# Kernel optimization log

Measured on AMD Instinct MI355X. Metric: run time of the kernel, lower is better.

Reference implementation:

```python
import jax, jax.numpy as jnp
import numpy as np

SR = 48000
TIME_LENGTH = 62400  # int(1.3 * 48000)
MAX_VOICES = 16


def _conv1d_same(x, k, b):
    # x: [B, L, Cin], k: [K, Cin, Cout] -> [B, L, Cout], keras Conv1D padding='same'
    y = jax.lax.conv_general_dilated(x, k, (1,), 'SAME', dimension_numbers=('NWC', 'WIO', 'NWC'))
    return y + b


def setup_inputs() -> dict:
    key = jax.random.key(0)
    ks = jax.random.split(key, 20)
    B, L, D, C = 16, 250, 128, 32
    V = MAX_VOICES
    din = D + C
    w = lambda k, s: jax.random.normal(k, s, jnp.float32) * 0.05
    inp = {}
    inp['base_signal'] = jax.random.normal(ks[0], (B, TIME_LENGTH), jnp.float32)
    inp['z'] = jax.random.normal(ks[1], (B, L, D), jnp.float32)
    inp['cond'] = jax.random.uniform(ks[2], (B, C), jnp.float32)
    inp['fundamental_freq'] = jax.random.uniform(ks[3], (B,), jnp.float32)
    # param_predictor: Dense(256)->Dense(128)->Dense(64)->Dense(4)
    inp['W1'] = w(ks[4], (din, 256)); inp['b1'] = jnp.zeros((256,), jnp.float32)
    inp['W2'] = w(ks[5], (256, 128)); inp['b2'] = jnp.zeros((128,), jnp.float32)
    inp['W3'] = w(ks[6], (128, 64));  inp['b3'] = jnp.zeros((64,), jnp.float32)
    inp['W4'] = w(ks[7], (64, 4));    inp['b4'] = jnp.zeros((4,), jnp.float32)
    # voice_gain_net: Conv1D(128,7)->Conv1D(64,5)->Conv1D(V,3), input channels = D + C
    inp['K1'] = w(ks[8], (7, din, 128)); inp['cb1'] = jnp.zeros((128,), jnp.float32)
    inp['K2'] = w(ks[9], (5, 128, 64));  inp['cb2'] = jnp.zeros((64,), jnp.float32)
    inp['K3'] = w(ks[10], (3, 64, V));   inp['cb3'] = jnp.zeros((V,), jnp.float32)
    return inp


def reference(base_signal, z, cond, fundamental_freq,
              W1, b1, W2, b2, W3, b3, W4, b4,
              K1, cb1, K2, cb2, K3, cb3):
    B, T = base_signal.shape
    L = z.shape[1]
    V = MAX_VOICES
    # ---- global param predictor ----
    z_global = jnp.mean(z, axis=1)
    x = jnp.concatenate([z_global, cond], axis=-1)
    h = jax.nn.relu(x @ W1 + b1)
    h = jax.nn.relu(h @ W2 + b2)
    h = jax.nn.relu(h @ W3 + b3)
    params = h @ W4 + b4  # [B,4]
    num_voices = 1.0 + 14.0 * jax.nn.sigmoid(params[:, 0:1])  # [B,1]
    detune_cents = params[:, 1:2] * 50.0                       # [B,1] (unused downstream, as in source)
    spread = jax.nn.sigmoid(params[:, 2:3])                    # [B,1]
    depth = jax.nn.sigmoid(params[:, 3:4]) * 0.5               # [B,1]
    # ---- per-voice gain envelopes at latent rate ----
    z_cond = jnp.concatenate([z, jnp.broadcast_to(cond[:, None, :], (B, L, cond.shape[-1]))], axis=-1)
    g = jax.nn.relu(_conv1d_same(z_cond, K1, cb1))
    g = jax.nn.relu(_conv1d_same(g, K2, cb2))
    g = _conv1d_same(g, K3, cb3)  # [B, L, V]
    # TF bilinear resize (half-pixel centers) L -> T along time axis
    scale = L / T
    src = jnp.clip((jnp.arange(T, dtype=jnp.float32) + 0.5) * scale - 0.5, 0.0, L - 1.0)
    i0 = jnp.floor(src).astype(jnp.int32)
    i1 = jnp.minimum(i0 + 1, L - 1)
    frac = (src - i0.astype(jnp.float32))[None, :, None]
    vg = g[:, i0, :] * (1.0 - frac) + g[:, i1, :] * frac
    voice_gains = jax.nn.softplus(vg)  # [B, T, V]
    # ---- 16-voice detune/roll/LFO-modulate/accumulate, vectorized over voices ----
    pos = (np.arange(V) - (V - 1) / 2.0) / V            # static [V]
    shifts = np.trunc(pos * 20.0).astype(np.int64)      # int() truncation as in source
    gidx = (np.arange(T)[None, :] - shifts[:, None]) % T  # static [V, T] gather for tf.roll
    shifted = base_signal[:, jnp.asarray(gidx)]         # [B, V, T]
    t = jnp.arange(T, dtype=jnp.float32) / SR
    lfo_freq = 3.0 + 0.3 * jnp.arange(V, dtype=jnp.float32)
    lfo = jnp.sin(2.0 * np.pi * lfo_freq[:, None] * t[None, :])  # [V, T]
    modulated = shifted * (1.0 + 0.2 * depth[:, 0][:, None, None] * lfo[None])  # [B, V, T]
    pan = 1.0 - jnp.abs(jnp.asarray(pos, dtype=jnp.float32))[None, :] * spread * 0.5  # [B, V]
    unison = jnp.einsum('bvt,btv,bv->bt', modulated, voice_gains, pan)  # [B, T]
    # ---- soft voice-count mask and normalization ----
    voice_mask = jax.nn.sigmoid((num_voices - jnp.arange(V, dtype=jnp.float32)[None, :]) * 2.0)  # [B, V]
    norm = jnp.sqrt(jnp.sum(voice_mask, axis=-1, keepdims=True) + 1e-6)  # [B, 1]
    gain_sum = jnp.einsum('btv,bv->bt', voice_gains, voice_mask)  # [B, T]
    return gain_sum / (norm + 1e-6) * unison
```

## Files before the change

kernel.cpp:

```cpp
#include <hip/hip_runtime.h>
#include <hip/hip_bf16.h>
#include <math.h>

#define L_LEN 250
#define D_DIM 128
#define C_DIM 32
#define DIN   160
#define NV    16
#define T_LEN 62400
#define CB    244

__global__ __launch_bounds__(256) void conv1_mlp_kernel(
        const float* __restrict__ z, const float* __restrict__ cond,
        const float* __restrict__ K1, float* __restrict__ parts1,
        const float* __restrict__ W1, const float* __restrict__ b1,
        const float* __restrict__ W2, const float* __restrict__ b2,
        const float* __restrict__ W3, const float* __restrict__ b3,
        const float* __restrict__ W4, const float* __restrict__ b4,
        float* __restrict__ P) {
    int tid = threadIdx.x;
    if (blockIdx.x < 16) {
        int b = blockIdx.x;
        __shared__ float xb[DIN];
        __shared__ float4 sm4[8][32];
        __shared__ float h1[256];
        __shared__ float h2[128];
        __shared__ float h3[64];
        __shared__ float pr[4];
        {
            int c4 = tid & 31, rg = tid >> 5;
            const float4* zp = (const float4*)(z + (size_t)b * L_LEN * D_DIM) + c4;
            float4 acc = make_float4(0.f, 0.f, 0.f, 0.f);
            for (int r = rg; r < L_LEN; r += 8) {
                float4 v = zp[(size_t)r * 32];
                acc.x += v.x; acc.y += v.y; acc.z += v.z; acc.w += v.w;
            }
            sm4[rg][c4] = acc;
        }
        __syncthreads();
        if (tid < 32) {
            float4 acc = sm4[0][tid];
            #pragma unroll
            for (int g = 1; g < 8; ++g) {
                float4 v = sm4[g][tid];
                acc.x += v.x; acc.y += v.y; acc.z += v.z; acc.w += v.w;
            }
            const float inv = 1.0f / (float)L_LEN;
            acc.x *= inv; acc.y *= inv; acc.z *= inv; acc.w *= inv;
            ((float4*)xb)[tid] = acc;
        } else if (tid >= 128 && tid < DIN) {
            xb[tid] = cond[b * C_DIM + (tid - 128)];
        }
        __syncthreads();
        {
            float a0 = b1[tid], a1 = 0.f;
            #pragma unroll 8
            for (int i = 0; i < DIN; i += 2) {
                a0 = fmaf(xb[i],     W1[i * 256 + tid],       a0);
                a1 = fmaf(xb[i + 1], W1[(i + 1) * 256 + tid], a1);
            }
            h1[tid] = fmaxf(a0 + a1, 0.f);
        }
        __syncthreads();
        if (tid < 128) {
            float a0 = b2[tid], a1 = 0.f;
            #pragma unroll 8
            for (int i = 0; i < 256; i += 2) {
                a0 = fmaf(h1[i],     W2[i * 128 + tid],       a0);
                a1 = fmaf(h1[i + 1], W2[(i + 1) * 128 + tid], a1);
            }
            h2[tid] = fmaxf(a0 + a1, 0.f);
        }
        __syncthreads();
        if (tid < 64) {
            float a0 = b3[tid], a1 = 0.f;
            #pragma unroll 8
            for (int i = 0; i < 128; i += 2) {
                a0 = fmaf(h2[i],     W3[i * 64 + tid],       a0);
                a1 = fmaf(h2[i + 1], W3[(i + 1) * 64 + tid], a1);
            }
            h3[tid] = fmaxf(a0 + a1, 0.f);
        }
        __syncthreads();
        if (tid < 4) {
            float acc = b4[tid];
            #pragma unroll 8
            for (int i = 0; i < 64; ++i) acc = fmaf(h3[i], W4[i * 4 + tid], acc);
            pr[tid] = acc;
        }
        __syncthreads();
        if (tid == 0) {
            float num_voices = 1.0f + 14.0f / (1.0f + __expf(-pr[0]));
            float spread     = 1.0f / (1.0f + __expf(-pr[2]));
            float depth      = 0.5f / (1.0f + __expf(-pr[3]));
            float* Pb = P + b * 40;
            float msum = 0.f;
            for (int v = 0; v < NV; ++v) {
                float m = 1.0f / (1.0f + __expf(-(num_voices - (float)v) * 2.0f));
                msum += m;
                Pb[2 + v] = m;
                float pos = ((float)v - 7.5f) * (1.0f / 16.0f);
                Pb[2 + NV + v] = 1.0f - fabsf(pos) * spread * 0.5f;
            }
            float norm = sqrtf(msum + 1e-6f);
            Pb[0] = depth;
            Pb[1] = 1.0f / (norm + 1e-6f);
        }
        return;
    }
    int blk = blockIdx.x - 16;
    int s  = blk >> 8;
    int b  = (blk >> 4) & 15;
    int lt = blk & 15;
    int l0 = lt * 16;
    __shared__ float smc[40][28];
    for (int idx = tid; idx < 22 * 40; idx += 256) {
        int pl = idx / 40;
        int il = idx - pl * 40;
        int p  = l0 - 3 + pl;
        int gi = s * 40 + il;
        float v = 0.f;
        if (p >= 0 && p < L_LEN)
            v = (gi < D_DIM) ? z[((size_t)b * L_LEN + p) * D_DIM + gi]
                             : cond[b * C_DIM + (gi - D_DIM)];
        smc[il][pl] = v;
    }
    __syncthreads();
    int oc = tid & 127;
    int lb = (tid >> 7) * 8;
    float acc[8];
    #pragma unroll
    for (int j = 0; j < 8; ++j) acc[j] = 0.f;
    const float* kbase = K1 + (size_t)(s * 40) * 128 + oc;
    for (int il = 0; il < 40; ++il) {
        float zr[16];
        *(float4*)&zr[0]  = *(const float4*)&smc[il][lb];
        *(float4*)&zr[4]  = *(const float4*)&smc[il][lb + 4];
        *(float4*)&zr[8]  = *(const float4*)&smc[il][lb + 8];
        *(float4*)&zr[12] = *(const float4*)&smc[il][lb + 12];
        const float* kp = kbase + (size_t)il * 128;
        #pragma unroll
        for (int tap = 0; tap < 7; ++tap) {
            float k = kp[(size_t)tap * DIN * 128];
            #pragma unroll
            for (int j = 0; j < 8; ++j) acc[j] = fmaf(zr[tap + j], k, acc[j]);
        }
    }
    float* po = parts1 + (size_t)s * (16 * L_LEN * 128) + ((size_t)b * L_LEN) * 128 + oc;
    #pragma unroll
    for (int j = 0; j < 8; ++j) {
        int l = l0 + lb + j;
        if (l < L_LEN) po[(size_t)l * 128] = acc[j];
    }
}

__global__ __launch_bounds__(256) void conv2_split_kernel(
        const float* __restrict__ parts1, const float* __restrict__ cb1,
        const float* __restrict__ K2, float* __restrict__ parts2) {
    int blk = blockIdx.x;
    int h  = blk >> 8;
    int b  = (blk >> 4) & 15;
    int lt = blk & 15;
    int l0 = lt * 16;
    int tid = threadIdx.x;
    const int PSTR = 16 * L_LEN * 128;
    __shared__ float sm[64][28];
    for (int idx = tid; idx < 20 * 64; idx += 256) {
        int pl = idx >> 6;
        int il = idx & 63;
        int p  = l0 - 2 + pl;
        int gi = h * 64 + il;
        float v = 0.f;
        if (p >= 0 && p < L_LEN) {
            size_t o = ((size_t)b * L_LEN + p) * 128 + gi;
            v = cb1[gi] + parts1[o] + parts1[o + PSTR] + parts1[o + 2 * PSTR] + parts1[o + 3 * PSTR];
            v = fmaxf(v, 0.f);
        }
        sm[il][pl] = v;
    }
    __syncthreads();
    int oc = tid & 63;
    int lb = (tid >> 6) * 4;
    float acc[4];
    #pragma unroll
    for (int j = 0; j < 4; ++j) acc[j] = 0.f;
    const float* kbase = K2 + (size_t)(h * 64) * 64 + oc;
    for (int il = 0; il < 64; ++il) {
        float zr[8];
        *(float4*)&zr[0] = *(const float4*)&sm[il][lb];
        *(float4*)&zr[4] = *(const float4*)&sm[il][lb + 4];
        const float* kp = kbase + (size_t)il * 64;
        #pragma unroll
        for (int tap = 0; tap < 5; ++tap) {
            float k = kp[(size_t)tap * 128 * 64];
            #pragma unroll
            for (int j = 0; j < 4; ++j) acc[j] = fmaf(zr[tap + j], k, acc[j]);
        }
    }
    float* po = parts2 + (size_t)h * (16 * L_LEN * 64) + ((size_t)b * L_LEN) * 64 + oc;
    #pragma unroll
    for (int j = 0; j < 4; ++j) {
        int l = l0 + lb + j;
        if (l < L_LEN) po[(size_t)l * 64] = acc[j];
    }
}

__global__ __launch_bounds__(256) void conv3_main_kernel(
        const float* __restrict__ base, const float* __restrict__ parts2,
        const float* __restrict__ cb2,
        const float* __restrict__ K3, const float* __restrict__ cb3,
        const float* __restrict__ P, float* __restrict__ out) {
    int b = blockIdx.x / CB;
    int c = blockIdx.x % CB;
    int t0 = c * 256;
    int tid = threadIdx.x;
    const int PSTR2 = 16 * L_LEN * 64;
    const float scale = 250.0f / 62400.0f;

    __shared__ float k3t[16][196];
    __shared__ float sA[6][68];
    __shared__ float g3loc[4][17];
    __shared__ float Pb[34];

    float src0 = ((float)t0 + 0.5f) * scale - 0.5f;
    src0 = fminf(fmaxf(src0, 0.0f), 249.0f);
    int L0 = (int)floorf(src0);

    if (tid < 34) Pb[tid] = P[b * 40 + tid];
    for (int idx = tid; idx < 3 * 64 * 16; idx += 256) {
        int v  = idx & 15;
        int ti = idx >> 4;
        k3t[v][ti] = K3[ti * 16 + v];
    }
    for (int idx = tid; idx < 6 * 64; idx += 256) {
        int pl = idx >> 6;
        int i  = idx & 63;
        int p  = L0 - 1 + pl;
        float v = 0.f;
        if (p >= 0 && p < L_LEN) {
            size_t o = ((size_t)b * L_LEN + p) * 64 + i;
            v = fmaxf(cb2[i] + parts2[o] + parts2[o + PSTR2], 0.f);
        }
        sA[pl][i] = v;
    }
    __syncthreads();

    {
        int seg = tid & 3;
        int v   = (tid >> 2) & 15;
        int r   = tid >> 6;
        float acc = 0.f;
        #pragma unroll
        for (int tap = 0; tap < 3; ++tap) {
            const float* gr = &sA[r + tap][seg * 16];
            const float* kr = &k3t[v][tap * 64 + seg * 16];
            #pragma unroll
            for (int j = 0; j < 4; ++j) {
                float4 g = *(const float4*)&gr[j * 4];
                float4 k = *(const float4*)&kr[j * 4];
                acc = fmaf(g.x, k.x, acc);
                acc = fmaf(g.y, k.y, acc);
                acc = fmaf(g.z, k.z, acc);
                acc = fmaf(g.w, k.w, acc);
            }
        }
        acc += __shfl_xor(acc, 1);
        acc += __shfl_xor(acc, 2);
        if (seg == 0) g3loc[r][v] = acc + cb3[v];
    }
    __syncthreads();

    int t = t0 + tid;
    if (t >= T_LEN) return;
    float depth = Pb[0];
    float coef  = Pb[1];
    float src = ((float)t + 0.5f) * scale - 0.5f;
    src = fminf(fmaxf(src, 0.0f), 249.0f);
    float fi0 = floorf(src);
    int i0 = (int)fi0;
    int i1 = min(i0 + 1, L_LEN - 1);
    float frac = src - fi0;
    int r0 = i0 - L0;
    int r1 = i1 - L0;
    float vg[16];
    #pragma unroll
    for (int v = 0; v < NV; ++v) {
        float a = g3loc[r0][v];
        float d = g3loc[r1][v];
        vg[v] = fmaf(d - a, frac, a);
    }
    float tsec = (float)t * (1.0f / 48000.0f);
    const float* bs = base + (size_t)b * T_LEN;
    const int shifts[NV] = {-9,-8,-6,-5,-4,-3,-1,0,0,1,3,4,5,6,8,9};
    float gain_sum = 0.f, uni = 0.f;
    #pragma unroll
    for (int v = 0; v < NV; ++v) {
        float x = vg[v];
        float sp = fmaxf(x, 0.f) + __logf(1.0f + __expf(-fabsf(x)));
        float fv = 3.0f + 0.3f * (float)v;
        float ph = fv * tsec;
        ph -= floorf(ph);
        float lfo = __builtin_amdgcn_sinf(ph);
        int tb = t - shifts[v];
        if (tb < 0) tb += T_LEN; else if (tb >= T_LEN) tb -= T_LEN;
        float mod = bs[tb] * fmaf(0.2f * depth, lfo, 1.0f);
        gain_sum = fmaf(sp, Pb[2 + v], gain_sum);
        uni      = fmaf(mod * sp, Pb[2 + NV + v], uni);
    }
    out[(size_t)b * T_LEN + t] = gain_sum * coef * uni;
}

__global__ void params_kernel(const float* __restrict__ z, const float* __restrict__ cond,
                              const float* __restrict__ W1, const float* __restrict__ b1,
                              const float* __restrict__ W2, const float* __restrict__ b2,
                              const float* __restrict__ W3, const float* __restrict__ b3,
                              const float* __restrict__ W4, const float* __restrict__ b4,
                              float* __restrict__ P) {
    int b = blockIdx.x;
    int tid = threadIdx.x;
    __shared__ float xb[DIN];
    __shared__ float zp2[128];
    __shared__ float h1[256];
    __shared__ float h2[128];
    __shared__ float h3[64];
    __shared__ float pr[4];
    {
        int i = tid & 127, half = tid >> 7;
        const float* zp = z + (size_t)b * L_LEN * D_DIM + i;
        float s = 0.f;
        for (int l = half; l < L_LEN; l += 2) s += zp[(size_t)l * D_DIM];
        if (half) zp2[i] = s;
        __syncthreads();
        if (!half) xb[i] = (s + zp2[i]) * (1.0f / (float)L_LEN);
        if (tid >= 128 && tid < DIN) xb[tid] = cond[b * C_DIM + (tid - 128)];
    }
    __syncthreads();
    {
        float acc = b1[tid];
        for (int i = 0; i < DIN; ++i) acc = fmaf(xb[i], W1[i * 256 + tid], acc);
        h1[tid] = fmaxf(acc, 0.f);
    }
    __syncthreads();
    if (tid < 128) {
        float acc = b2[tid];
        for (int i = 0; i < 256; ++i) acc = fmaf(h1[i], W2[i * 128 + tid], acc);
        h2[tid] = fmaxf(acc, 0.f);
    }
    __syncthreads();
    if (tid < 64) {
        float acc = b3[tid];
        for (int i = 0; i < 128; ++i) acc = fmaf(h2[i], W3[i * 64 + tid], acc);
        h3[tid] = fmaxf(acc, 0.f);
    }
    __syncthreads();
    if (tid < 4) {
        float acc = b4[tid];
        for (int i = 0; i < 64; ++i) acc = fmaf(h3[i], W4[i * 4 + tid], acc);
        pr[tid] = acc;
    }
    __syncthreads();
    if (tid == 0) {
        float num_voices = 1.0f + 14.0f / (1.0f + __expf(-pr[0]));
        float spread     = 1.0f / (1.0f + __expf(-pr[2]));
        float depth      = 0.5f / (1.0f + __expf(-pr[3]));
        float* Pb = P + b * 40;
        float msum = 0.f;
        for (int v = 0; v < NV; ++v) {
            float m = 1.0f / (1.0f + __expf(-(num_voices - (float)v) * 2.0f));
            msum += m;
            Pb[2 + v] = m;
            float pos = ((float)v - 7.5f) * (1.0f / 16.0f);
            Pb[2 + NV + v] = 1.0f - fabsf(pos) * spread * 0.5f;
        }
        float norm = sqrtf(msum + 1e-6f);
        Pb[0] = depth;
        Pb[1] = 1.0f / (norm + 1e-6f);
    }
}

__global__ void conv1_mono_kernel(const float* __restrict__ z, const float* __restrict__ cond,
                                  const float* __restrict__ K1, const float* __restrict__ cb1,
                                  float* __restrict__ g1) {
    int b  = blockIdx.x >> 4;
    int lt = blockIdx.x & 15;
    int l0 = lt * 16;
    int tid = threadIdx.x;
    __shared__ float sm[DIN][22];
    for (int idx = tid; idx < 22 * DIN; idx += 256) {
        int pl = idx / DIN;
        int i  = idx - pl * DIN;
        int p  = l0 - 3 + pl;
        float v = 0.f;
        if (p >= 0 && p < L_LEN)
            v = (i < D_DIM) ? z[((size_t)b * L_LEN + p) * D_DIM + i]
                            : cond[b * C_DIM + (i - D_DIM)];
        sm[i][pl] = v;
    }
    __syncthreads();
    int oc = tid & 127;
    int lb = (tid >> 7) * 8;
    float bias = cb1[oc];
    float acc[8];
    #pragma unroll
    for (int j = 0; j < 8; ++j) acc[j] = bias;
    for (int i = 0; i < DIN; ++i) {
        float zr[14];
        #pragma unroll
        for (int q = 0; q < 14; ++q) zr[q] = sm[i][lb + q];
        #pragma unroll
        for (int tap = 0; tap < 7; ++tap) {
            float k = K1[(size_t)(tap * DIN + i) * 128 + oc];
            #pragma unroll
            for (int j = 0; j < 8; ++j) acc[j] = fmaf(zr[tap + j], k, acc[j]);
        }
    }
    #pragma unroll
    for (int j = 0; j < 8; ++j) {
        int l = l0 + lb + j;
        if (l < L_LEN) g1[((size_t)b * L_LEN + l) * 128 + oc] = fmaxf(acc[j], 0.f);
    }
}

__global__ void conv2_mono_kernel(const float* __restrict__ g1,
                                  const float* __restrict__ K2, const float* __restrict__ cb2,
                                  float* __restrict__ g2) {
    int b  = blockIdx.x >> 4;
    int lt = blockIdx.x & 15;
    int l0 = lt * 16;
    int tid = threadIdx.x;
    __shared__ float sm[128][20];
    for (int idx = tid; idx < 20 * 128; idx += 256) {
        int pl = idx >> 7;
        int i  = idx & 127;
        int p  = l0 - 2 + pl;
        float v = (p >= 0 && p < L_LEN) ? g1[((size_t)b * L_LEN + p) * 128 + i] : 0.f;
        sm[i][pl] = v;
    }
    __syncthreads();
    int oc = tid & 63;
    int lb = (tid >> 6) * 4;
    float bias = cb2[oc];
    float acc[4];
    #pragma unroll
    for (int j = 0; j < 4; ++j) acc[j] = bias;
    for (int i = 0; i < 128; ++i) {
        float zr[8];
        #pragma unroll
        for (int q = 0; q < 8; ++q) zr[q] = sm[i][lb + q];
        #pragma unroll
        for (int tap = 0; tap < 5; ++tap) {
            float k = K2[(size_t)(tap * 128 + i) * 64 + oc];
            #pragma unroll
            for (int j = 0; j < 4; ++j) acc[j] = fmaf(zr[tap + j], k, acc[j]);
        }
    }
    #pragma unroll
    for (int j = 0; j < 4; ++j) {
        int l = l0 + lb + j;
        if (l < L_LEN) g2[((size_t)b * L_LEN + l) * 64 + oc] = fmaxf(acc[j], 0.f);
    }
}

__global__ void conv3_mono_kernel(const float* __restrict__ g2,
                                  const float* __restrict__ K3, const float* __restrict__ cb3,
                                  float* __restrict__ g3) {
    int b  = blockIdx.x >> 4;
    int lt = blockIdx.x & 15;
    int l0 = lt * 16;
    int tid = threadIdx.x;
    int v  = tid & 15;
    int ll = tid >> 4;
    int l  = l0 + ll;
    if (l >= L_LEN) return;
    float acc = cb3[v];
    #pragma unroll
    for (int tap = 0; tap < 3; ++tap) {
        int p = l + tap - 1;
        if (p < 0 || p >= L_LEN) continue;
        const float* gp = g2 + ((size_t)b * L_LEN + p) * 64;
        #pragma unroll
        for (int i = 0; i < 64; ++i) acc = fmaf(gp[i], K3[(size_t)(tap * 64 + i) * 16 + v], acc);
    }
    g3[((size_t)b * L_LEN + l) * 16 + v] = acc;
}

__global__ __launch_bounds__(256) void main_mono_kernel(
        const float* __restrict__ base, const float* __restrict__ g3,
        const float* __restrict__ P, float* __restrict__ out) {
    int b = blockIdx.x / CB;
    int c = blockIdx.x % CB;
    int t = c * 256 + threadIdx.x;
    __shared__ float Pb[34];
    if (threadIdx.x < 34) Pb[threadIdx.x] = P[b * 40 + threadIdx.x];
    __syncthreads();
    if (t >= T_LEN) return;
    float depth = Pb[0];
    float coef  = Pb[1];
    const float scale = 250.0f / 62400.0f;
    float src = ((float)t + 0.5f) * scale - 0.5f;
    src = fminf(fmaxf(src, 0.0f), 249.0f);
    float fi0 = floorf(src);
    int i0 = (int)fi0;
    int i1 = min(i0 + 1, L_LEN - 1);
    float frac = src - fi0;
    const float4* r0 = (const float4*)(g3 + ((size_t)b * L_LEN + i0) * NV);
    const float4* r1 = (const float4*)(g3 + ((size_t)b * L_LEN + i1) * NV);
    float vg[16];
    #pragma unroll
    for (int q = 0; q < 4; ++q) {
        float4 a = r0[q];
        float4 d = r1[q];
        vg[q * 4 + 0] = fmaf(d.x - a.x, frac, a.x);
        vg[q * 4 + 1] = fmaf(d.y - a.y, frac, a.y);
        vg[q * 4 + 2] = fmaf(d.z - a.z, frac, a.z);
        vg[q * 4 + 3] = fmaf(d.w - a.w, frac, a.w);
    }
    float tsec = (float)t * (1.0f / 48000.0f);
    const float* bs = base + (size_t)b * T_LEN;
    const int shifts[NV] = {-9,-8,-6,-5,-4,-3,-1,0,0,1,3,4,5,6,8,9};
    float gain_sum = 0.f, uni = 0.f;
    #pragma unroll
    for (int v = 0; v < NV; ++v) {
        float x = vg[v];
        float sp = fmaxf(x, 0.f) + __logf(1.0f + __expf(-fabsf(x)));
        float fv = 3.0f + 0.3f * (float)v;
        float ph = fv * tsec;
        ph -= floorf(ph);
        float lfo = __builtin_amdgcn_sinf(ph);
        int tb = t - shifts[v];
        if (tb < 0) tb += T_LEN; else if (tb >= T_LEN) tb -= T_LEN;
        float mod = bs[tb] * fmaf(0.2f * depth, lfo, 1.0f);
        gain_sum = fmaf(sp, Pb[2 + v], gain_sum);
        uni      = fmaf(mod * sp, Pb[2 + NV + v], uni);
    }
    out[(size_t)b * T_LEN + t] = gain_sum * coef * uni;
}

extern "C" void kernel_launch(void* const* d_in, const int* in_sizes, int n_in,
                              void* d_out, int out_size, void* d_ws, size_t ws_size,
                              hipStream_t stream) {
    const float* base = (const float*)d_in[0];
    const float* z    = (const float*)d_in[1];
    const float* cond = (const float*)d_in[2];
    const float* W1 = (const float*)d_in[4];  const float* b1 = (const float*)d_in[5];
    const float* W2 = (const float*)d_in[6];  const float* b2 = (const float*)d_in[7];
    const float* W3 = (const float*)d_in[8];  const float* b3 = (const float*)d_in[9];
    const float* W4 = (const float*)d_in[10]; const float* b4 = (const float*)d_in[11];
    const float* K1 = (const float*)d_in[12]; const float* cb1 = (const float*)d_in[13];
    const float* K2 = (const float*)d_in[14]; const float* cb2 = (const float*)d_in[15];
    const float* K3 = (const float*)d_in[16]; const float* cb3 = (const float*)d_in[17];
    float* out = (float*)d_out;

    int B = in_sizes[0] / T_LEN;

    float* ws = (float*)d_ws;
    const size_t P1 = (size_t)16 * L_LEN * 128;
    const size_t P2 = (size_t)16 * L_LEN * 64;
    size_t need = (1024 + 4 * P1 + 2 * P2) * sizeof(float);

    float* P = ws;
    if (ws_size >= need) {
        float* parts1 = ws + 1024;
        float* parts2 = parts1 + 4 * P1;
        conv1_mlp_kernel<<<16 + 4 * B * 16, 256, 0, stream>>>(
            z, cond, K1, parts1, W1, b1, W2, b2, W3, b3, W4, b4, P);
        conv2_split_kernel<<<2 * B * 16, 256, 0, stream>>>(parts1, cb1, K2, parts2);
        conv3_main_kernel<<<B * CB, 256, 0, stream>>>(base, parts2, cb2, K3, cb3, P, out);
    } else {
        float* g1 = ws + 1024;
        float* g2 = g1 + (size_t)B * L_LEN * 128;
        float* g3 = g2 + (size_t)B * L_LEN * 64;
        params_kernel<<<B, 256, 0, stream>>>(z, cond, W1, b1, W2, b2, W3, b3, W4, b4, P);
        conv1_mono_kernel<<<B * 16, 256, 0, stream>>>(z, cond, K1, cb1, g1);
        conv2_mono_kernel<<<B * 16, 256, 0, stream>>>(g1, K2, cb2, g2);
        conv3_mono_kernel<<<B * 16, 256, 0, stream>>>(g2, K3, cb3, g3);
        main_mono_kernel<<<B * CB, 256, 0, stream>>>(base, g3, P, out);
    }
}
```

Measured before the change: 65.28 us.

## Register-tile conv1/conv2 over output channel pairs and split conv2 input four ways

Conv1 and conv2 now give each thread two adjacent output channels and fewer positions. Weights are loaded as float2 and two input channels are processed per iteration, so each shared-memory input value feeds more FMAs. Conv2 splits its input channels four ways instead of two, doubling its block count for more parallelism. Conv3 therefore sums four partial buffers, and the workspace requirement grows.

```diff
diff --git a/kernel.cpp b/kernel.cpp
--- a/kernel.cpp
+++ b/kernel.cpp
@@ -113,7 +113,7 @@
     int b  = (blk >> 4) & 15;
     int lt = blk & 15;
     int l0 = lt * 16;
-    __shared__ float smc[40][28];
+    __shared__ float smc[40][24];
     for (int idx = tid; idx < 22 * 40; idx += 256) {
         int pl = idx / 40;
         int il = idx - pl * 40;
@@ -126,31 +126,44 @@
         smc[il][pl] = v;
     }
     __syncthreads();
-    int oc = tid & 127;
-    int lb = (tid >> 7) * 8;
-    float acc[8];
-    #pragma unroll
-    for (int j = 0; j < 8; ++j) acc[j] = 0.f;
-    const float* kbase = K1 + (size_t)(s * 40) * 128 + oc;
-    for (int il = 0; il < 40; ++il) {
-        float zr[16];
-        *(float4*)&zr[0]  = *(const float4*)&smc[il][lb];
-        *(float4*)&zr[4]  = *(const float4*)&smc[il][lb + 4];
-        *(float4*)&zr[8]  = *(const float4*)&smc[il][lb + 8];
-        *(float4*)&zr[12] = *(const float4*)&smc[il][lb + 12];
-        const float* kp = kbase + (size_t)il * 128;
+    int oc0   = (tid & 63) << 1;
+    int lbase = (tid >> 6) * 4;
+    float acc[2][4];
+    #pragma unroll
+    for (int j = 0; j < 4; ++j) { acc[0][j] = 0.f; acc[1][j] = 0.f; }
+    const float* kb = K1 + (size_t)(s * 40) * 128 + oc0;
+    for (int il = 0; il < 40; il += 2) {
+        float2 w0[7], w1[7];
         #pragma unroll
         for (int tap = 0; tap < 7; ++tap) {
-            float k = kp[(size_t)tap * DIN * 128];
+            const float* k0 = kb + ((size_t)tap * DIN + il) * 128;
+            w0[tap] = *(const float2*)(k0);
+            w1[tap] = *(const float2*)(k0 + 128);
+        }
+        float zr0[10], zr1[10];
+        *(float4*)&zr0[0] = *(const float4*)&smc[il][lbase];
+        *(float4*)&zr0[4] = *(const float4*)&smc[il][lbase + 4];
+        *(float2*)&zr0[8] = *(const float2*)&smc[il][lbase + 8];
+        *(float4*)&zr1[0] = *(const float4*)&smc[il + 1][lbase];
+        *(float4*)&zr1[4] = *(const float4*)&smc[il + 1][lbase + 4];
+        *(float2*)&zr1[8] = *(const float2*)&smc[il + 1][lbase + 8];
+        #pragma unroll
+        for (int tap = 0; tap < 7; ++tap) {
             #pragma unroll
-            for (int j = 0; j < 8; ++j) acc[j] = fmaf(zr[tap + j], k, acc[j]);
-        }
-    }
-    float* po = parts1 + (size_t)s * (16 * L_LEN * 128) + ((size_t)b * L_LEN) * 128 + oc;
-    #pragma unroll
-    for (int j = 0; j < 8; ++j) {
-        int l = l0 + lb + j;
-        if (l < L_LEN) po[(size_t)l * 128] = acc[j];
+            for (int j = 0; j < 4; ++j) {
+                acc[0][j] = fmaf(zr0[tap + j], w0[tap].x, acc[0][j]);
+                acc[1][j] = fmaf(zr0[tap + j], w0[tap].y, acc[1][j]);
+                acc[0][j] = fmaf(zr1[tap + j], w1[tap].x, acc[0][j]);
+                acc[1][j] = fmaf(zr1[tap + j], w1[tap].y, acc[1][j]);
+            }
+        }
+    }
+    float* po = parts1 + (size_t)s * (16 * L_LEN * 128)
+              + ((size_t)b * L_LEN + l0 + lbase) * 128 + oc0;
+    #pragma unroll
+    for (int j = 0; j < 4; ++j) {
+        int l = l0 + lbase + j;
+        if (l < L_LEN) *(float2*)(po + (size_t)j * 128) = make_float2(acc[0][j], acc[1][j]);
     }
 }
 
@@ -158,18 +171,18 @@
         const float* __restrict__ parts1, const float* __restrict__ cb1,
         const float* __restrict__ K2, float* __restrict__ parts2) {
     int blk = blockIdx.x;
-    int h  = blk >> 8;
+    int s  = blk >> 8;
     int b  = (blk >> 4) & 15;
     int lt = blk & 15;
     int l0 = lt * 16;
     int tid = threadIdx.x;
     const int PSTR = 16 * L_LEN * 128;
-    __shared__ float sm[64][28];
-    for (int idx = tid; idx < 20 * 64; idx += 256) {
-        int pl = idx >> 6;
-        int il = idx & 63;
+    __shared__ float sm[32][24];
+    for (int idx = tid; idx < 20 * 32; idx += 256) {
+        int pl = idx >> 5;
+        int il = idx & 31;
         int p  = l0 - 2 + pl;
-        int gi = h * 64 + il;
+        int gi = s * 32 + il;
         float v = 0.f;
         if (p >= 0 && p < L_LEN) {
             size_t o = ((size_t)b * L_LEN + p) * 128 + gi;
@@ -179,29 +192,42 @@
         sm[il][pl] = v;
     }
     __syncthreads();
-    int oc = tid & 63;
-    int lb = (tid >> 6) * 4;
-    float acc[4];
-    #pragma unroll
-    for (int j = 0; j < 4; ++j) acc[j] = 0.f;
-    const float* kbase = K2 + (size_t)(h * 64) * 64 + oc;
-    for (int il = 0; il < 64; ++il) {
-        float zr[8];
-        *(float4*)&zr[0] = *(const float4*)&sm[il][lb];
-        *(float4*)&zr[4] = *(const float4*)&sm[il][lb + 4];
-        const float* kp = kbase + (size_t)il * 64;
+    int oc0   = (tid & 31) << 1;
+    int lbase = (tid >> 5) * 2;
+    float acc[2][2];
+    acc[0][0] = acc[0][1] = acc[1][0] = acc[1][1] = 0.f;
+    const float* kb = K2 + (size_t)(s * 32) * 64 + oc0;
+    for (int il = 0; il < 32; il += 2) {
+        float2 w0[5], w1[5];
         #pragma unroll
         for (int tap = 0; tap < 5; ++tap) {
-            float k = kp[(size_t)tap * 128 * 64];
+            const float* k0 = kb + ((size_t)tap * 128 + il) * 64;
+            w0[tap] = *(const float2*)(k0);
+            w1[tap] = *(const float2*)(k0 + 64);
+        }
+        float zr0[6], zr1[6];
+        #pragma unroll
+        for (int q = 0; q < 6; q += 2) {
+            *(float2*)&zr0[q] = *(const float2*)&sm[il][lbase + q];
+            *(float2*)&zr1[q] = *(const float2*)&sm[il + 1][lbase + q];
+        }
+        #pragma unroll
+        for (int tap = 0; tap < 5; ++tap) {
             #pragma unroll
-            for (int j = 0; j < 4; ++j) acc[j] = fmaf(zr[tap + j], k, acc[j]);
-        }
-    }
-    float* po = parts2 + (size_t)h * (16 * L_LEN * 64) + ((size_t)b * L_LEN) * 64 + oc;
-    #pragma unroll
-    for (int j = 0; j < 4; ++j) {
-        int l = l0 + lb + j;
-        if (l < L_LEN) po[(size_t)l * 64] = acc[j];
+            for (int j = 0; j < 2; ++j) {
+                acc[0][j] = fmaf(zr0[tap + j], w0[tap].x, acc[0][j]);
+                acc[1][j] = fmaf(zr0[tap + j], w0[tap].y, acc[1][j]);
+                acc[0][j] = fmaf(zr1[tap + j], w1[tap].x, acc[0][j]);
+                acc[1][j] = fmaf(zr1[tap + j], w1[tap].y, acc[1][j]);
+            }
+        }
+    }
+    float* po = parts2 + (size_t)s * (16 * L_LEN * 64)
+              + ((size_t)b * L_LEN + l0 + lbase) * 64 + oc0;
+    #pragma unroll
+    for (int j = 0; j < 2; ++j) {
+        int l = l0 + lbase + j;
+        if (l < L_LEN) *(float2*)(po + (size_t)j * 64) = make_float2(acc[0][j], acc[1][j]);
     }
 }
 
@@ -239,7 +265,8 @@
         float v = 0.f;
         if (p >= 0 && p < L_LEN) {
             size_t o = ((size_t)b * L_LEN + p) * 64 + i;
-            v = fmaxf(cb2[i] + parts2[o] + parts2[o + PSTR2], 0.f);
+            v = fmaxf(cb2[i] + parts2[o] + parts2[o + PSTR2]
+                             + parts2[o + 2 * PSTR2] + parts2[o + 3 * PSTR2], 0.f);
         }
         sA[pl][i] = v;
     }
@@ -556,7 +583,7 @@
     float* ws = (float*)d_ws;
     const size_t P1 = (size_t)16 * L_LEN * 128;
     const size_t P2 = (size_t)16 * L_LEN * 64;
-    size_t need = (1024 + 4 * P1 + 2 * P2) * sizeof(float);
+    size_t need = (1024 + 4 * P1 + 4 * P2) * sizeof(float);
 
     float* P = ws;
     if (ws_size >= need) {
@@ -564,7 +591,7 @@
         float* parts2 = parts1 + 4 * P1;
         conv1_mlp_kernel<<<16 + 4 * B * 16, 256, 0, stream>>>(
             z, cond, K1, parts1, W1, b1, W2, b2, W3, b3, W4, b4, P);
-        conv2_split_kernel<<<2 * B * 16, 256, 0, stream>>>(parts1, cb1, K2, parts2);
+        conv2_split_kernel<<<4 * B * 16, 256, 0, stream>>>(parts1, cb1, K2, parts2);
         conv3_main_kernel<<<B * CB, 256, 0, stream>>>(base, parts2, cb2, K3, cb3, P, out);
     } else {
         float* g1 = ws + 1024;
```

Result: slower. 210.4 us (+222.2%).

## Stage conv weights in shared memory and retile conv1/conv2 by output-channel quarter

Applied to the files above, without the earlier changes.

Conv1 and conv2 blocks now cover a slice of 32 output channels over a longer sequence span, and load the matching weight slice into shared memory, transposed so each thread reads taps contiguously. Previously every thread fetched weights from global memory inside the inner loop. Each conv1 thread now accumulates 16 positions instead of 8, which raises per-thread reuse of the input rows. The trade-offs are much larger shared-memory footprints that may lower occupancy, grid sizes hardcoded for B=16, and redundant weight loads across blocks.

```diff
diff --git a/kernel.cpp b/kernel.cpp
--- a/kernel.cpp
+++ b/kernel.cpp
@@ -19,14 +19,17 @@
         const float* __restrict__ W4, const float* __restrict__ b4,
         float* __restrict__ P) {
     int tid = threadIdx.x;
+    __shared__ float kw[7 * 40 * 32];
+    __shared__ float smc[40][136];
+
     if (blockIdx.x < 16) {
         int b = blockIdx.x;
-        __shared__ float xb[DIN];
-        __shared__ float4 sm4[8][32];
-        __shared__ float h1[256];
-        __shared__ float h2[128];
-        __shared__ float h3[64];
-        __shared__ float pr[4];
+        float* xb = kw;
+        float* h1 = kw + 160;
+        float* h2 = kw + 416;
+        float* h3 = kw + 544;
+        float* pr = kw + 608;
+        float4* sm4 = (float4*)(kw + 640);
         {
             int c4 = tid & 31, rg = tid >> 5;
             const float4* zp = (const float4*)(z + (size_t)b * L_LEN * D_DIM) + c4;
@@ -35,14 +38,14 @@
                 float4 v = zp[(size_t)r * 32];
                 acc.x += v.x; acc.y += v.y; acc.z += v.z; acc.w += v.w;
             }
-            sm4[rg][c4] = acc;
+            sm4[rg * 32 + c4] = acc;
         }
         __syncthreads();
         if (tid < 32) {
-            float4 acc = sm4[0][tid];
+            float4 acc = sm4[tid];
             #pragma unroll
             for (int g = 1; g < 8; ++g) {
-                float4 v = sm4[g][tid];
+                float4 v = sm4[g * 32 + tid];
                 acc.x += v.x; acc.y += v.y; acc.z += v.z; acc.w += v.w;
             }
             const float inv = 1.0f / (float)L_LEN;
@@ -109,12 +112,21 @@
         return;
     }
     int blk = blockIdx.x - 16;
-    int s  = blk >> 8;
-    int b  = (blk >> 4) & 15;
-    int lt = blk & 15;
-    int l0 = lt * 16;
-    __shared__ float smc[40][28];
-    for (int idx = tid; idx < 22 * 40; idx += 256) {
+    int s  = blk >> 7;
+    int q  = (blk >> 5) & 3;
+    int b  = (blk >> 1) & 15;
+    int lh = blk & 1;
+    int l0 = lh * 125;
+
+    for (int idx = tid; idx < 7 * 40 * 32; idx += 256) {
+        int tap = idx / (40 * 32);
+        int rem = idx - tap * (40 * 32);
+        int ic  = rem >> 5;
+        int oc  = rem & 31;
+        kw[(ic * 7 + tap) * 32 + oc] =
+            K1[((size_t)tap * DIN + s * 40 + ic) * 128 + q * 32 + oc];
+    }
+    for (int idx = tid; idx < 134 * 40; idx += 256) {
         int pl = idx / 40;
         int il = idx - pl * 40;
         int p  = l0 - 3 + pl;
@@ -126,78 +138,93 @@
         smc[il][pl] = v;
     }
     __syncthreads();
-    int oc = tid & 127;
-    int lb = (tid >> 7) * 8;
-    float acc[8];
-    #pragma unroll
-    for (int j = 0; j < 8; ++j) acc[j] = 0.f;
-    const float* kbase = K1 + (size_t)(s * 40) * 128 + oc;
-    for (int il = 0; il < 40; ++il) {
-        float zr[16];
-        *(float4*)&zr[0]  = *(const float4*)&smc[il][lb];
-        *(float4*)&zr[4]  = *(const float4*)&smc[il][lb + 4];
-        *(float4*)&zr[8]  = *(const float4*)&smc[il][lb + 8];
-        *(float4*)&zr[12] = *(const float4*)&smc[il][lb + 12];
-        const float* kp = kbase + (size_t)il * 128;
+
+    int oc = tid & 31;
+    int lb = (tid >> 5) << 4;
+    float acc[16];
+    #pragma unroll
+    for (int j = 0; j < 16; ++j) acc[j] = 0.f;
+    #pragma unroll 2
+    for (int ic = 0; ic < 40; ++ic) {
+        float zr[22];
+        #pragma unroll
+        for (int qq = 0; qq < 20; qq += 4)
+            *(float4*)&zr[qq] = *(const float4*)&smc[ic][lb + qq];
+        *(float2*)&zr[20] = *(const float2*)&smc[ic][lb + 20];
+        const float* kwp = &kw[ic * 7 * 32 + oc];
         #pragma unroll
         for (int tap = 0; tap < 7; ++tap) {
-            float k = kp[(size_t)tap * DIN * 128];
+            float w = kwp[tap * 32];
             #pragma unroll
-            for (int j = 0; j < 8; ++j) acc[j] = fmaf(zr[tap + j], k, acc[j]);
-        }
-    }
-    float* po = parts1 + (size_t)s * (16 * L_LEN * 128) + ((size_t)b * L_LEN) * 128 + oc;
-    #pragma unroll
-    for (int j = 0; j < 8; ++j) {
-        int l = l0 + lb + j;
-        if (l < L_LEN) po[(size_t)l * 128] = acc[j];
+            for (int j = 0; j < 16; ++j)
+                acc[j] = fmaf(zr[tap + j], w, acc[j]);
+        }
+    }
+    float* po = parts1 + (size_t)s * (16 * L_LEN * 128)
+              + ((size_t)b * L_LEN) * 128 + q * 32 + oc;
+    #pragma unroll
+    for (int j = 0; j < 16; ++j) {
+        int ll = lb + j;
+        int l  = l0 + ll;
+        if (ll < 125 && l < L_LEN) po[(size_t)l * 128] = acc[j];
     }
 }
 
 __global__ __launch_bounds__(256) void conv2_split_kernel(
         const float* __restrict__ parts1, const float* __restrict__ cb1,
         const float* __restrict__ K2, float* __restrict__ parts2) {
-    int blk = blockIdx.x;
-    int h  = blk >> 8;
-    int b  = (blk >> 4) & 15;
-    int lt = blk & 15;
-    int l0 = lt * 16;
+    int s  = blockIdx.x >> 8;
+    int q  = (blockIdx.x >> 7) & 1;
+    int b  = (blockIdx.x >> 3) & 15;
+    int lt = blockIdx.x & 7;
+    int l0 = lt * 32;
     int tid = threadIdx.x;
     const int PSTR = 16 * L_LEN * 128;
-    __shared__ float sm[64][28];
-    for (int idx = tid; idx < 20 * 64; idx += 256) {
+    __shared__ float kw[5 * 64 * 32];
+    __shared__ float smr[64][40];
+    for (int idx = tid; idx < 5 * 64 * 32; idx += 256) {
+        int tap = idx / (64 * 32);
+        int rem = idx - tap * (64 * 32);
+        int ic  = rem >> 5;
+        int oc  = rem & 31;
+        kw[(ic * 5 + tap) * 32 + oc] =
+            K2[((size_t)tap * 128 + s * 64 + ic) * 64 + q * 32 + oc];
+    }
+    for (int idx = tid; idx < 36 * 64; idx += 256) {
         int pl = idx >> 6;
         int il = idx & 63;
         int p  = l0 - 2 + pl;
-        int gi = h * 64 + il;
+        int gi = s * 64 + il;
         float v = 0.f;
         if (p >= 0 && p < L_LEN) {
             size_t o = ((size_t)b * L_LEN + p) * 128 + gi;
             v = cb1[gi] + parts1[o] + parts1[o + PSTR] + parts1[o + 2 * PSTR] + parts1[o + 3 * PSTR];
             v = fmaxf(v, 0.f);
         }
-        sm[il][pl] = v;
-    }
-    __syncthreads();
-    int oc = tid & 63;
-    int lb = (tid >> 6) * 4;
+        smr[il][pl] = v;
+    }
+    __syncthreads();
+    int oc = tid & 31;
+    int lb = (tid >> 5) << 2;
     float acc[4];
     #pragma unroll
     for (int j = 0; j < 4; ++j) acc[j] = 0.f;
-    const float* kbase = K2 + (size_t)(h * 64) * 64 + oc;
-    for (int il = 0; il < 64; ++il) {
+    #pragma unroll 4
+    for (int ic = 0; ic < 64; ++ic) {
         float zr[8];
-        *(float4*)&zr[0] = *(const float4*)&sm[il][lb];
-        *(float4*)&zr[4] = *(const float4*)&sm[il][lb + 4];
-        const float* kp = kbase + (size_t)il * 64;
+        *(float4*)&zr[0] = *(const float4*)&smr[ic][lb];
+        *(float4*)&zr[4] = *(const float4*)&smr[ic][lb + 4];
+        const float* kwp = &kw[ic * 5 * 32 + oc];
         #pragma unroll
         for (int tap = 0; tap < 5; ++tap) {
-            float k = kp[(size_t)tap * 128 * 64];
+            float w = kwp[tap * 32];
             #pragma unroll
-            for (int j = 0; j < 4; ++j) acc[j] = fmaf(zr[tap + j], k, acc[j]);
-        }
-    }
-    float* po = parts2 + (size_t)h * (16 * L_LEN * 64) + ((size_t)b * L_LEN) * 64 + oc;
+            for (int j = 0; j < 4; ++j)
+                acc[j] = fmaf(zr[tap + j], w, acc[j]);
+        }
+    }
+    float* po = parts2 + (size_t)s * (16 * L_LEN * 64)
+              + ((size_t)b * L_LEN) * 64 + q * 32 + oc;
     #pragma unroll
     for (int j = 0; j < 4; ++j) {
         int l = l0 + lb + j;
@@ -562,9 +589,9 @@
     if (ws_size >= need) {
         float* parts1 = ws + 1024;
         float* parts2 = parts1 + 4 * P1;
-        conv1_mlp_kernel<<<16 + 4 * B * 16, 256, 0, stream>>>(
+        conv1_mlp_kernel<<<16 + 512, 256, 0, stream>>>(
             z, cond, K1, parts1, W1, b1, W2, b2, W3, b3, W4, b4, P);
-        conv2_split_kernel<<<2 * B * 16, 256, 0, stream>>>(parts1, cb1, K2, parts2);
+        conv2_split_kernel<<<512, 256, 0, stream>>>(parts1, cb1, K2, parts2);
         conv3_main_kernel<<<B * CB, 256, 0, stream>>>(base, parts2, cb2, K3, cb3, P, out);
     } else {
         float* g1 = ws + 1024;
```

New measurement: 82.14 us. 25.8% more time.
